# Optimization experiments

Measured on AMD Instinct MI355X. Metric: run time of the kernel, lower is better.

The kernel has to match this reference:

```python
import jax, jax.numpy as jnp
import numpy as np
from jax import lax

B, T, D = 8, 4096, 1024


def setup_inputs() -> dict:
    key = jax.random.key(0)
    ks = jax.random.split(key, 8)
    s = 1.0 / np.sqrt(D)  # keep GEMM outputs O(1)
    return {
        "x": jax.random.normal(ks[0], (B, T, D), dtype=jnp.float32),
        "state_p": jnp.zeros((B, D), dtype=jnp.float32),
        "decay": 0.8 + 0.19 * jax.random.uniform(ks[1], (D,), dtype=jnp.float32),  # ~0.9, stable
        "mass": jnp.ones((D,), dtype=jnp.float32),
        "Wq": s * jax.random.normal(ks[2], (D, D), dtype=jnp.float32),
        "bq": jnp.zeros((D,), dtype=jnp.float32),
        "Wk": s * jax.random.normal(ks[3], (D, D), dtype=jnp.float32),
        "bk": jnp.zeros((D,), dtype=jnp.float32),
        "Wv": s * jax.random.normal(ks[4], (D, D), dtype=jnp.float32),
        "bv": jnp.zeros((D,), dtype=jnp.float32),
    }


def reference(x, state_p, decay, mass, Wq, bq, Wk, bk, Wv, bv):
    # Batch all per-timestep projections into single GEMMs over (B*T) tokens.
    k_logit = jnp.einsum("btd,ed->bte", x, Wk) + bk        # [B,T,D]
    v = jnp.einsum("btd,ed->bte", x, Wv) + bv              # [B,T,D]
    u = jax.nn.sigmoid(k_logit) * v                          # gated input, [B,T,D]

    # Diagonal linear recurrence p_t = decay * p_{t-1} + u_t via scan over time.
    def step(p, u_t):
        p = p * decay + u_t
        return p, p

    final_p, ps = lax.scan(step, state_p, jnp.swapaxes(u, 0, 1))  # ps: [T,B,D]
    p = jnp.swapaxes(ps, 0, 1)                                     # [B,T,D]

    velocities = (jnp.einsum("btd,ed->bte", p, Wq) + bq) / mass    # [B,T,D]
    return velocities, final_p
```

## Files before the change

### kernel.cpp

```cpp
#include <hip/hip_runtime.h>
#include <stdint.h>
#include <stddef.h>

#define D_DIM 1024
#define T_LEN 4096
#define B_SZ 8
#define M_ROWS 32768
#define KTOT 1024
#define CHUNK 64
#define NCHUNK 64

typedef unsigned short u16;
typedef unsigned short u16x8 __attribute__((ext_vector_type(8)));
typedef __bf16 bf16x8 __attribute__((ext_vector_type(8)));
typedef float f32x4 __attribute__((ext_vector_type(4)));

__device__ __forceinline__ u16 f2bf(float f) {
    union { float f; unsigned u; } v; v.f = f;
    unsigned r = v.u + 0x7fffu + ((v.u >> 16) & 1u);
    return (u16)(r >> 16);
}
__device__ __forceinline__ float bf2f(u16 h) {
    union { unsigned u; float f; } v; v.u = ((unsigned)h) << 16;
    return v.f;
}

__global__ void convert_kernel(const float* __restrict__ src, u16* __restrict__ dst, int n4) {
    int i = blockIdx.x * blockDim.x + threadIdx.x;
    int stride = gridDim.x * blockDim.x;
    for (int j = i; j < n4; j += stride) {
        float4 v = ((const float4*)src)[j];
        ushort4 o;
        o.x = f2bf(v.x); o.y = f2bf(v.y); o.z = f2bf(v.z); o.w = f2bf(v.w);
        ((ushort4*)dst)[j] = o;
    }
}

__global__ void convert3_kernel(const float* __restrict__ s0, const float* __restrict__ s1,
                                const float* __restrict__ s2,
                                u16* __restrict__ d0, u16* __restrict__ d1, u16* __restrict__ d2,
                                int n4each) {
    int i = blockIdx.x * blockDim.x + threadIdx.x;
    int total = 3 * n4each;
    int stride = gridDim.x * blockDim.x;
    for (int j = i; j < total; j += stride) {
        int which = j / n4each;
        int off = j - which * n4each;
        const float* s = which == 0 ? s0 : (which == 1 ? s1 : s2);
        u16* d = which == 0 ? d0 : (which == 1 ? d1 : d2);
        float4 v = ((const float4*)s)[off];
        ushort4 o;
        o.x = f2bf(v.x); o.y = f2bf(v.y); o.z = f2bf(v.z); o.w = f2bf(v.w);
        ((ushort4*)d)[off] = o;
    }
}

__device__ __forceinline__ void gload16(const u16* g, u16* l) {
    __builtin_amdgcn_global_load_lds(
        (const __attribute__((address_space(1))) void*)g,
        (__attribute__((address_space(3))) void*)l,
        16, 0, 0);
}

template<bool DUAL>
__global__ __launch_bounds__(512, 2) void gemm3_kernel(
    const u16* __restrict__ A,
    const u16* __restrict__ B0g,
    const u16* __restrict__ B1g,
    const float* __restrict__ bias0,
    const float* __restrict__ bias1,
    u16* __restrict__ Uout,
    float* __restrict__ Fout)
{
    constexpr int BM = 256;
    constexpr int BN = DUAL ? 128 : 256;
    constexpr int MFR = DUAL ? 4 : 8;
    constexpr int BUF = 16384;
    constexpr int NT = KTOT / 32;

    __shared__ u16 smem[4 * BUF];

    const int tid  = threadIdx.x;
    const int w    = tid >> 6;
    const int lane = tid & 63;

    const int cpx = gridDim.x >> 3;
    const int bid = blockIdx.x;
    const int swz = (bid & 7) * cpx + (bid >> 3);

    const int nCol = D_DIM / BN;
    const int M0 = (swz / nCol) * BM;
    const int N0 = (swz % nCol) * BM / (BM / BN);

    const int srow  = lane >> 2;
    const int sslot = lane & 3;
    const int sg    = sslot ^ ((srow >> 1) & 3);

    const u16* pA0 = A + (size_t)(M0 + (w * 2 + 0) * 16 + srow) * KTOT + sg * 8;
    const u16* pA1 = A + (size_t)(M0 + (w * 2 + 1) * 16 + srow) * KTOT + sg * 8;
    const u16* pB0a;
    const u16* pB0b = nullptr;
    const u16* pB1a = nullptr;
    if (DUAL) {
        pB0a = B0g + (size_t)(N0 + w * 16 + srow) * KTOT + sg * 8;
        pB1a = B1g + (size_t)(N0 + w * 16 + srow) * KTOT + sg * 8;
    } else {
        pB0a = B0g + (size_t)(N0 + (w * 2 + 0) * 16 + srow) * KTOT + sg * 8;
        pB0b = B0g + (size_t)(N0 + (w * 2 + 1) * 16 + srow) * KTOT + sg * 8;
    }

    auto stageA = [&](int buf) {
        u16* s = smem + buf * BUF;
        gload16(pA0, s + (w * 2 + 0) * 512); pA0 += 32;
        gload16(pA1, s + (w * 2 + 1) * 512); pA1 += 32;
    };
    auto stageB = [&](int buf) {
        u16* s = smem + buf * BUF;
        if (DUAL) {
            gload16(pB0a, s + 8192 + w * 512);  pB0a += 32;
            gload16(pB1a, s + 12288 + w * 512); pB1a += 32;
        } else {
            gload16(pB0a, s + 8192 + (w * 2 + 0) * 512); pB0a += 32;
            gload16(pB0b, s + 8192 + (w * 2 + 1) * 512); pB0b += 32;
        }
    };

    const int wrow = DUAL ? (w >> 1) * 64 : (w >> 2) * 128;
    const int wcol = DUAL ? (w & 1) * 64 : (w & 3) * 64;
    const int fr = lane & 15;
    const int fq = lane >> 4;

    int offA[MFR], offB[4];
#pragma unroll
    for (int m = 0; m < MFR; ++m) {
        int row = wrow + m * 16 + fr;
        offA[m] = row * 32 + ((fq ^ ((row >> 1) & 3)) << 3);
    }
#pragma unroll
    for (int n = 0; n < 4; ++n) {
        int row = wcol + n * 16 + fr;
        offB[n] = row * 32 + ((fq ^ ((row >> 1) & 3)) << 3);
    }

    f32x4 acc0[MFR][4] = {};
    f32x4 acc1[DUAL ? MFR : 1][4] = {};

    stageA(0); stageB(0); stageA(1); stageB(1); stageA(2); stageB(2);

    for (int kt = 0; kt < NT; ++kt) {
        if (kt < NT - 2)       asm volatile("s_waitcnt vmcnt(8)" ::: "memory");
        else if (kt == NT - 2) asm volatile("s_waitcnt vmcnt(4)" ::: "memory");
        else                   asm volatile("s_waitcnt vmcnt(0)" ::: "memory");
        __builtin_amdgcn_s_barrier();

        const u16* As  = smem + (kt & 3) * BUF;
        const u16* Bs0 = As + 8192;
        const u16* Bs1 = As + 12288;

        bf16x8 af[MFR], b0f[4], b1f[4];

#pragma unroll
        for (int m = 0; m < 4; ++m)
            af[m] = *(const bf16x8*)(As + offA[m]);
#pragma unroll
        for (int n = 0; n < 4; ++n)
            b0f[n] = *(const bf16x8*)(Bs0 + offB[n]);
        if (kt + 3 < NT) stageA((kt + 3) & 3);
        asm volatile("s_waitcnt lgkmcnt(0)" ::: "memory");
        __builtin_amdgcn_sched_barrier(0);
        __builtin_amdgcn_s_setprio(1);
#pragma unroll
        for (int m = 0; m < 4; ++m)
#pragma unroll
            for (int n = 0; n < 4; ++n)
                acc0[m][n] = __builtin_amdgcn_mfma_f32_16x16x32_bf16(af[m], b0f[n], acc0[m][n], 0, 0, 0);
        __builtin_amdgcn_s_setprio(0);
        __builtin_amdgcn_sched_barrier(0);

        __builtin_amdgcn_s_barrier();
        if (DUAL) {
#pragma unroll
            for (int n = 0; n < 4; ++n)
                b1f[n] = *(const bf16x8*)(Bs1 + offB[n]);
        } else {
#pragma unroll
            for (int m = 4; m < MFR; ++m)
                af[m] = *(const bf16x8*)(As + offA[m]);
        }
        if (kt + 3 < NT) stageB((kt + 3) & 3);
        asm volatile("s_waitcnt lgkmcnt(0)" ::: "memory");
        __builtin_amdgcn_sched_barrier(0);
        __builtin_amdgcn_s_setprio(1);
        if (DUAL) {
#pragma unroll
            for (int m = 0; m < 4; ++m)
#pragma unroll
                for (int n = 0; n < 4; ++n)
                    acc1[m][n] = __builtin_amdgcn_mfma_f32_16x16x32_bf16(af[m], b1f[n], acc1[m][n], 0, 0, 0);
        } else {
#pragma unroll
            for (int m = 4; m < MFR; ++m)
#pragma unroll
                for (int n = 0; n < 4; ++n)
                    acc0[m][n] = __builtin_amdgcn_mfma_f32_16x16x32_bf16(af[m], b0f[n], acc0[m][n], 0, 0, 0);
        }
        __builtin_amdgcn_s_setprio(0);
        __builtin_amdgcn_sched_barrier(0);
    }

#pragma unroll
    for (int n = 0; n < 4; ++n) {
        int col = N0 + wcol + n * 16 + fr;
        float b0 = bias0[col];
        float b1 = bias1[col];
#pragma unroll
        for (int m = 0; m < MFR; ++m) {
            int row0 = M0 + wrow + m * 16 + fq * 4;
#pragma unroll
            for (int j = 0; j < 4; ++j) {
                if (DUAL) {
                    float kl = acc0[m][n][j] + b0;
                    float vv = acc1[m][n][j] + b1;
                    float sg2 = 1.0f / (1.0f + __expf(-kl));
                    Uout[(size_t)(row0 + j) * D_DIM + col] = f2bf(sg2 * vv);
                } else {
                    Fout[(size_t)(row0 + j) * D_DIM + col] = (acc0[m][n][j] + b0) / b1;
                }
            }
        }
    }
}

__global__ void chunk_carry_kernel(const u16* __restrict__ u, const float* __restrict__ decay,
                                   float* __restrict__ localc) {
    int id = blockIdx.x * blockDim.x + threadIdx.x;
    int d8 = id & 127;
    int c  = (id >> 7) & (NCHUNK - 1);
    int b  = id >> 13;
    float4 dlo = ((const float4*)decay)[d8 * 2];
    float4 dhi = ((const float4*)decay)[d8 * 2 + 1];
    float dec[8] = {dlo.x, dlo.y, dlo.z, dlo.w, dhi.x, dhi.y, dhi.z, dhi.w};
    float carry[8] = {};
    const u16* up = u + ((size_t)b * T_LEN + (size_t)c * CHUNK) * D_DIM + d8 * 8;
    for (int s = 0; s < CHUNK; ++s) {
        u16x8 v = *(const u16x8*)(up + (size_t)s * D_DIM);
#pragma unroll
        for (int j = 0; j < 8; ++j)
            carry[j] = fmaf(carry[j], dec[j], bf2f(v[j]));
    }
    float* lc = localc + ((size_t)(b * NCHUNK + c)) * D_DIM + d8 * 8;
#pragma unroll
    for (int j = 0; j < 8; ++j) lc[j] = carry[j];
}

__global__ void carry_scan_kernel(const float* __restrict__ localc, const float* __restrict__ state_p,
                                  const float* __restrict__ decay, float* __restrict__ prefix,
                                  float* __restrict__ final_p) {
    int id = blockIdx.x * blockDim.x + threadIdx.x;
    int d = id & (D_DIM - 1);
    int b = id >> 10;
    float dec = decay[d];
    float dl = dec;
#pragma unroll
    for (int i = 0; i < 6; ++i) dl *= dl;
    float P = state_p[id];
    for (int c = 0; c < NCHUNK; ++c) {
        int idx = (b * NCHUNK + c) * D_DIM + d;
        prefix[idx] = P;
        P = fmaf(P, dl, localc[idx]);
    }
    final_p[id] = P;
}

__global__ void reconstruct_kernel(u16* __restrict__ u, const float* __restrict__ decay,
                                   const float* __restrict__ prefix) {
    int id = blockIdx.x * blockDim.x + threadIdx.x;
    int d8 = id & 127;
    int c  = (id >> 7) & (NCHUNK - 1);
    int b  = id >> 13;
    float4 dlo = ((const float4*)decay)[d8 * 2];
    float4 dhi = ((const float4*)decay)[d8 * 2 + 1];
    float dec[8] = {dlo.x, dlo.y, dlo.z, dlo.w, dhi.x, dhi.y, dhi.z, dhi.w};
    const float* pf = prefix + ((size_t)(b * NCHUNK + c)) * D_DIM + d8 * 8;
    float p[8];
#pragma unroll
    for (int j = 0; j < 8; ++j) p[j] = pf[j];
    u16* up = u + ((size_t)b * T_LEN + (size_t)c * CHUNK) * D_DIM + d8 * 8;
    for (int s = 0; s < CHUNK; ++s) {
        u16x8 v = *(const u16x8*)(up + (size_t)s * D_DIM);
        u16x8 o;
#pragma unroll
        for (int j = 0; j < 8; ++j) {
            p[j] = fmaf(p[j], dec[j], bf2f(v[j]));
            o[j] = f2bf(p[j]);
        }
        *(u16x8*)(up + (size_t)s * D_DIM) = o;
    }
}

extern "C" void kernel_launch(void* const* d_in, const int* in_sizes, int n_in,
                              void* d_out, int out_size, void* d_ws, size_t ws_size,
                              hipStream_t stream) {
    const float* x       = (const float*)d_in[0];
    const float* state_p = (const float*)d_in[1];
    const float* decay   = (const float*)d_in[2];
    const float* mass    = (const float*)d_in[3];
    const float* Wq      = (const float*)d_in[4];
    const float* bq      = (const float*)d_in[5];
    const float* Wk      = (const float*)d_in[6];
    const float* bk      = (const float*)d_in[7];
    const float* Wv      = (const float*)d_in[8];
    const float* bv      = (const float*)d_in[9];

    float* out     = (float*)d_out;
    float* final_p = out + (size_t)M_ROWS * D_DIM;

    u16* xb = (u16*)d_out;

    u16* wkb = (u16*)d_ws;
    u16* wvb = wkb + 1048576;
    u16* wqb = wvb + 1048576;
    u16* ub  = wqb + 1048576;
    float* localc = (float*)(ub + (size_t)M_ROWS * D_DIM);
    float* prefix = localc + B_SZ * NCHUNK * D_DIM;

    convert_kernel<<<4096, 256, 0, stream>>>(x, xb, (M_ROWS * D_DIM) / 4);
    convert3_kernel<<<1024, 256, 0, stream>>>(Wk, Wv, Wq, wkb, wvb, wqb, (D_DIM * D_DIM) / 4);

    gemm3_kernel<true><<<dim3(1024), dim3(512), 0, stream>>>(
        xb, wkb, wvb, bk, bv, ub, nullptr);

    chunk_carry_kernel<<<256, 256, 0, stream>>>(ub, decay, localc);
    carry_scan_kernel<<<32, 256, 0, stream>>>(localc, state_p, decay, prefix, final_p);
    reconstruct_kernel<<<256, 256, 0, stream>>>(ub, decay, prefix);

    gemm3_kernel<false><<<dim3(512), dim3(512), 0, stream>>>(
        ub, wqb, nullptr, bq, mass, nullptr, out);
}
```

Measured before the change: 306.4 us.

## Software-pipeline LDS fragment loads across k-steps with ping-pong register buffers

Restructures the GEMM main loop so the A and B0 fragments for the next k-tile are read from LDS during the current tile's second MFMA phase. Two register sets alternate between tiles, and partial lgkmcnt waits replace full drains. The goal is to hide LDS read latency behind MFMA work. In exchange it raises register pressure under launch_bounds(512,2), and the vmcnt and barrier ordering changes could race if miscounted.

```diff
diff --git a/kernel.cpp b/kernel.cpp
--- a/kernel.cpp
+++ b/kernel.cpp
@@ -63,7 +63,7 @@
 }
 
 template<bool DUAL>
-__global__ __launch_bounds__(512, 2) void gemm3_kernel(
+__global__ __launch_bounds__(512, 2) void gemm4_kernel(
     const u16* __restrict__ A,
     const u16* __restrict__ B0g,
     const u16* __restrict__ B1g,
@@ -90,7 +90,7 @@
 
     const int nCol = D_DIM / BN;
     const int M0 = (swz / nCol) * BM;
-    const int N0 = (swz % nCol) * BM / (BM / BN);
+    const int N0 = (swz % nCol) * BN;
 
     const int srow  = lane >> 2;
     const int sslot = lane & 3;
@@ -143,70 +143,75 @@
     }
 
     f32x4 acc0[MFR][4] = {};
-    f32x4 acc1[DUAL ? MFR : 1][4] = {};
+    f32x4 acc1[DUAL ? 4 : 1][4] = {};
+    bf16x8 af0[MFR], af1[MFR], b00[4], b01[4];
+    bf16x8 b1f[DUAL ? 4 : 1];
 
     stageA(0); stageB(0); stageA(1); stageB(1); stageA(2); stageB(2);
-
-    for (int kt = 0; kt < NT; ++kt) {
-        if (kt < NT - 2)       asm volatile("s_waitcnt vmcnt(8)" ::: "memory");
-        else if (kt == NT - 2) asm volatile("s_waitcnt vmcnt(4)" ::: "memory");
-        else                   asm volatile("s_waitcnt vmcnt(0)" ::: "memory");
-        __builtin_amdgcn_s_barrier();
-
-        const u16* As  = smem + (kt & 3) * BUF;
-        const u16* Bs0 = As + 8192;
-        const u16* Bs1 = As + 12288;
-
-        bf16x8 af[MFR], b0f[4], b1f[4];
-
-#pragma unroll
-        for (int m = 0; m < 4; ++m)
-            af[m] = *(const bf16x8*)(As + offA[m]);
-#pragma unroll
-        for (int n = 0; n < 4; ++n)
-            b0f[n] = *(const bf16x8*)(Bs0 + offB[n]);
-        if (kt + 3 < NT) stageA((kt + 3) & 3);
-        asm volatile("s_waitcnt lgkmcnt(0)" ::: "memory");
-        __builtin_amdgcn_sched_barrier(0);
-        __builtin_amdgcn_s_setprio(1);
-#pragma unroll
-        for (int m = 0; m < 4; ++m)
-#pragma unroll
-            for (int n = 0; n < 4; ++n)
-                acc0[m][n] = __builtin_amdgcn_mfma_f32_16x16x32_bf16(af[m], b0f[n], acc0[m][n], 0, 0, 0);
-        __builtin_amdgcn_s_setprio(0);
-        __builtin_amdgcn_sched_barrier(0);
-
-        __builtin_amdgcn_s_barrier();
-        if (DUAL) {
-#pragma unroll
-            for (int n = 0; n < 4; ++n)
-                b1f[n] = *(const bf16x8*)(Bs1 + offB[n]);
-        } else {
-#pragma unroll
-            for (int m = 4; m < MFR; ++m)
-                af[m] = *(const bf16x8*)(As + offA[m]);
-        }
-        if (kt + 3 < NT) stageB((kt + 3) & 3);
-        asm volatile("s_waitcnt lgkmcnt(0)" ::: "memory");
-        __builtin_amdgcn_sched_barrier(0);
-        __builtin_amdgcn_s_setprio(1);
-        if (DUAL) {
-#pragma unroll
-            for (int m = 0; m < 4; ++m)
-#pragma unroll
-                for (int n = 0; n < 4; ++n)
-                    acc1[m][n] = __builtin_amdgcn_mfma_f32_16x16x32_bf16(af[m], b1f[n], acc1[m][n], 0, 0, 0);
-        } else {
-#pragma unroll
-            for (int m = 4; m < MFR; ++m)
-#pragma unroll
-                for (int n = 0; n < 4; ++n)
-                    acc0[m][n] = __builtin_amdgcn_mfma_f32_16x16x32_bf16(af[m], b0f[n], acc0[m][n], 0, 0, 0);
-        }
-        __builtin_amdgcn_s_setprio(0);
-        __builtin_amdgcn_sched_barrier(0);
-    }
+    asm volatile("s_waitcnt vmcnt(8)" ::: "memory");
+    __builtin_amdgcn_s_barrier();
+#pragma unroll
+    for (int m = 0; m < 4; ++m) af0[m] = *(const bf16x8*)(smem + offA[m]);
+#pragma unroll
+    for (int n = 0; n < 4; ++n) b00[n] = *(const bf16x8*)(smem + 8192 + offB[n]);
+
+#define PHASES(KT, AFC, B0C, AFN, B0N)                                               \
+  {                                                                                  \
+    const int kt_ = (KT);                                                            \
+    if (kt_ < NT - 2) { asm volatile("s_waitcnt vmcnt(4)" ::: "memory"); }           \
+    else              { asm volatile("s_waitcnt vmcnt(0)" ::: "memory"); }           \
+    __builtin_amdgcn_sched_barrier(0);                                               \
+    const u16* As_ = smem + (kt_ & 3) * BUF;                                         \
+    if constexpr (DUAL) {                                                            \
+      _Pragma("unroll") for (int n = 0; n < 4; ++n)                                  \
+        b1f[n] = *(const bf16x8*)(As_ + 12288 + offB[n]);                            \
+    } else {                                                                         \
+      _Pragma("unroll") for (int m = 4; m < MFR; ++m)                                \
+        AFC[m] = *(const bf16x8*)(As_ + offA[m]);                                    \
+    }                                                                                \
+    if (kt_ + 3 < NT) stageA((kt_ + 3) & 3);                                         \
+    __builtin_amdgcn_sched_barrier(0);                                               \
+    __builtin_amdgcn_s_barrier();                                                    \
+    asm volatile("s_waitcnt lgkmcnt(4)" ::: "memory");                               \
+    __builtin_amdgcn_sched_barrier(0);                                               \
+    __builtin_amdgcn_s_setprio(1);                                                   \
+    _Pragma("unroll") for (int m = 0; m < 4; ++m)                                    \
+      _Pragma("unroll") for (int n = 0; n < 4; ++n)                                  \
+        acc0[m][n] = __builtin_amdgcn_mfma_f32_16x16x32_bf16(AFC[m], B0C[n], acc0[m][n], 0, 0, 0); \
+    __builtin_amdgcn_s_setprio(0);                                                   \
+    __builtin_amdgcn_sched_barrier(0);                                               \
+    __builtin_amdgcn_s_barrier();                                                    \
+    const u16* Asn_ = smem + ((kt_ + 1) & 3) * BUF;                                  \
+    _Pragma("unroll") for (int m = 0; m < 4; ++m)                                    \
+      AFN[m] = *(const bf16x8*)(Asn_ + offA[m]);                                     \
+    _Pragma("unroll") for (int n = 0; n < 4; ++n)                                    \
+      B0N[n] = *(const bf16x8*)(Asn_ + 8192 + offB[n]);                              \
+    if (kt_ + 3 < NT) stageB((kt_ + 3) & 3);                                         \
+    __builtin_amdgcn_sched_barrier(0);                                               \
+    __builtin_amdgcn_s_barrier();                                                    \
+    asm volatile("s_waitcnt lgkmcnt(8)" ::: "memory");                               \
+    __builtin_amdgcn_sched_barrier(0);                                               \
+    __builtin_amdgcn_s_setprio(1);                                                   \
+    if constexpr (DUAL) {                                                            \
+      _Pragma("unroll") for (int m = 0; m < 4; ++m)                                  \
+        _Pragma("unroll") for (int n = 0; n < 4; ++n)                                \
+          acc1[m][n] = __builtin_amdgcn_mfma_f32_16x16x32_bf16(AFC[m], b1f[n], acc1[m][n], 0, 0, 0); \
+    } else {                                                                         \
+      _Pragma("unroll") for (int m = 4; m < MFR; ++m)                                \
+        _Pragma("unroll") for (int n = 0; n < 4; ++n)                                \
+          acc0[m][n] = __builtin_amdgcn_mfma_f32_16x16x32_bf16(AFC[m], B0C[n], acc0[m][n], 0, 0, 0); \
+    }                                                                                \
+    __builtin_amdgcn_s_setprio(0);                                                   \
+    __builtin_amdgcn_sched_barrier(0);                                               \
+    __builtin_amdgcn_s_barrier();                                                    \
+  }
+
+#pragma unroll 1
+    for (int kt = 0; kt < NT; kt += 2) {
+        PHASES(kt,     af0, b00, af1, b01);
+        PHASES(kt + 1, af1, b01, af0, b00);
+    }
+#undef PHASES
 
 #pragma unroll
     for (int n = 0; n < 4; ++n) {
@@ -327,13 +332,13 @@
     convert_kernel<<<4096, 256, 0, stream>>>(x, xb, (M_ROWS * D_DIM) / 4);
     convert3_kernel<<<1024, 256, 0, stream>>>(Wk, Wv, Wq, wkb, wvb, wqb, (D_DIM * D_DIM) / 4);
 
-    gemm3_kernel<true><<<dim3(1024), dim3(512), 0, stream>>>(
+    gemm4_kernel<true><<<dim3(1024), dim3(512), 0, stream>>>(
         xb, wkb, wvb, bk, bv, ub, nullptr);
 
     chunk_carry_kernel<<<256, 256, 0, stream>>>(ub, decay, localc);
     carry_scan_kernel<<<32, 256, 0, stream>>>(localc, state_p, decay, prefix, final_p);
     reconstruct_kernel<<<256, 256, 0, stream>>>(ub, decay, prefix);
 
-    gemm3_kernel<false><<<dim3(512), dim3(512), 0, stream>>>(
+    gemm4_kernel<false><<<dim3(512), dim3(512), 0, stream>>>(
         ub, wqb, nullptr, bq, mass, nullptr, out);
 }
```

Result: no change. 310.4 us (+1.3%).

## Interleave Wk/Wv into one weight matrix and use a 64-deep double-buffered GEMM

Applied to the files above, without the earlier changes.

Wk and Wv are interleaved in 16-row groups into one concatenated bf16 weight matrix. The first GEMM then runs as a single 256x256 tile GEMM whose epilogue pairs adjacent k/v fragments to apply sigmoid gating, replacing the separate dual-B path. The GEMM pipeline changes from a 4-stage, 32-wide K buffer ring to 2 buffers of 64-wide K, split into four half-steps with more barriers. This is meant to cut barrier/wait overhead per K element and unify tile shapes, but it trades prefetch depth for larger stages, which risks exposing memory latency.

```diff
diff --git a/kernel.cpp b/kernel.cpp
--- a/kernel.cpp
+++ b/kernel.cpp
@@ -36,22 +36,26 @@
     }
 }
 
-__global__ void convert3_kernel(const float* __restrict__ s0, const float* __restrict__ s1,
-                                const float* __restrict__ s2,
-                                u16* __restrict__ d0, u16* __restrict__ d1, u16* __restrict__ d2,
-                                int n4each) {
-    int i = blockIdx.x * blockDim.x + threadIdx.x;
-    int total = 3 * n4each;
+__global__ void convert_w_kernel(const float* __restrict__ Wk, const float* __restrict__ Wv,
+                                 const float* __restrict__ Wq,
+                                 u16* __restrict__ wcat, u16* __restrict__ wqb) {
+    int total = 3072 * 256;
     int stride = gridDim.x * blockDim.x;
-    for (int j = i; j < total; j += stride) {
-        int which = j / n4each;
-        int off = j - which * n4each;
-        const float* s = which == 0 ? s0 : (which == 1 ? s1 : s2);
-        u16* d = which == 0 ? d0 : (which == 1 ? d1 : d2);
-        float4 v = ((const float4*)s)[off];
+    for (int idx = blockIdx.x * blockDim.x + threadIdx.x; idx < total; idx += stride) {
+        int r = idx >> 8, c4 = idx & 255;
+        const float* src; u16* dst;
+        if (r < 2048) {
+            int g = r >> 5, j = r & 31;
+            src = (j < 16 ? Wk : Wv) + (size_t)(g * 16 + (j & 15)) * D_DIM;
+            dst = wcat + (size_t)r * D_DIM;
+        } else {
+            src = Wq + (size_t)(r - 2048) * D_DIM;
+            dst = wqb + (size_t)(r - 2048) * D_DIM;
+        }
+        float4 v = ((const float4*)src)[c4];
         ushort4 o;
         o.x = f2bf(v.x); o.y = f2bf(v.y); o.z = f2bf(v.z); o.w = f2bf(v.w);
-        ((ushort4*)d)[off] = o;
+        ((ushort4*)dst)[c4] = o;
     }
 }
 
@@ -62,110 +66,98 @@
         16, 0, 0);
 }
 
-template<bool DUAL>
-__global__ __launch_bounds__(512, 2) void gemm3_kernel(
+template<bool CAT>
+__global__ __launch_bounds__(512, 2) void gemm5_kernel(
     const u16* __restrict__ A,
-    const u16* __restrict__ B0g,
-    const u16* __restrict__ B1g,
+    const u16* __restrict__ Bg,
     const float* __restrict__ bias0,
     const float* __restrict__ bias1,
     u16* __restrict__ Uout,
     float* __restrict__ Fout)
 {
-    constexpr int BM = 256;
-    constexpr int BN = DUAL ? 128 : 256;
-    constexpr int MFR = DUAL ? 4 : 8;
-    constexpr int BUF = 16384;
-    constexpr int NT = KTOT / 32;
-
-    __shared__ u16 smem[4 * BUF];
+    constexpr int NT = KTOT / 64;
+    __shared__ u16 smem[2 * 32768];
 
     const int tid  = threadIdx.x;
     const int w    = tid >> 6;
     const int lane = tid & 63;
 
     const int cpx = gridDim.x >> 3;
-    const int bid = blockIdx.x;
-    const int swz = (bid & 7) * cpx + (bid >> 3);
-
-    const int nCol = D_DIM / BN;
-    const int M0 = (swz / nCol) * BM;
-    const int N0 = (swz % nCol) * BM / (BM / BN);
-
-    const int srow  = lane >> 2;
-    const int sslot = lane & 3;
-    const int sg    = sslot ^ ((srow >> 1) & 3);
-
-    const u16* pA0 = A + (size_t)(M0 + (w * 2 + 0) * 16 + srow) * KTOT + sg * 8;
-    const u16* pA1 = A + (size_t)(M0 + (w * 2 + 1) * 16 + srow) * KTOT + sg * 8;
-    const u16* pB0a;
-    const u16* pB0b = nullptr;
-    const u16* pB1a = nullptr;
-    if (DUAL) {
-        pB0a = B0g + (size_t)(N0 + w * 16 + srow) * KTOT + sg * 8;
-        pB1a = B1g + (size_t)(N0 + w * 16 + srow) * KTOT + sg * 8;
-    } else {
-        pB0a = B0g + (size_t)(N0 + (w * 2 + 0) * 16 + srow) * KTOT + sg * 8;
-        pB0b = B0g + (size_t)(N0 + (w * 2 + 1) * 16 + srow) * KTOT + sg * 8;
-    }
-
-    auto stageA = [&](int buf) {
-        u16* s = smem + buf * BUF;
-        gload16(pA0, s + (w * 2 + 0) * 512); pA0 += 32;
-        gload16(pA1, s + (w * 2 + 1) * 512); pA1 += 32;
+    const int swz = (blockIdx.x & 7) * cpx + (blockIdx.x >> 3);
+    const int nCol = CAT ? 8 : 4;
+    const int M0 = (swz / nCol) * 256;
+    const int N0 = (swz % nCol) * 256;
+
+    const int srow = lane >> 2;
+    const int sg   = (lane & 3) ^ ((srow >> 1) & 3);
+
+    const u16* pA0 = A  + (size_t)(M0 + w * 32 +      srow) * KTOT + sg * 8;
+    const u16* pA1 = A  + (size_t)(M0 + w * 32 + 16 + srow) * KTOT + sg * 8;
+    const u16* pB0 = Bg + (size_t)(N0 + w * 32 +      srow) * KTOT + sg * 8;
+    const u16* pB1 = Bg + (size_t)(N0 + w * 32 + 16 + srow) * KTOT + sg * 8;
+
+    auto stA = [&](u16* nxt, int h) {
+        gload16(pA0, nxt + h * 8192 + w * 1024);       pA0 += 32;
+        gload16(pA1, nxt + h * 8192 + w * 1024 + 512); pA1 += 32;
     };
-    auto stageB = [&](int buf) {
-        u16* s = smem + buf * BUF;
-        if (DUAL) {
-            gload16(pB0a, s + 8192 + w * 512);  pB0a += 32;
-            gload16(pB1a, s + 12288 + w * 512); pB1a += 32;
-        } else {
-            gload16(pB0a, s + 8192 + (w * 2 + 0) * 512); pB0a += 32;
-            gload16(pB0b, s + 8192 + (w * 2 + 1) * 512); pB0b += 32;
-        }
+    auto stB = [&](u16* nxt, int h) {
+        gload16(pB0, nxt + 16384 + h * 8192 + w * 1024);       pB0 += 32;
+        gload16(pB1, nxt + 16384 + h * 8192 + w * 1024 + 512); pB1 += 32;
     };
 
-    const int wrow = DUAL ? (w >> 1) * 64 : (w >> 2) * 128;
-    const int wcol = DUAL ? (w & 1) * 64 : (w & 3) * 64;
+    const int wrow = (w >> 2) * 128;
+    const int wcol = (w & 3) * 64;
     const int fr = lane & 15;
     const int fq = lane >> 4;
 
-    int offA[MFR], offB[4];
-#pragma unroll
-    for (int m = 0; m < MFR; ++m) {
+    int offA[8], offB[4];
+#pragma unroll
+    for (int m = 0; m < 8; ++m) {
         int row = wrow + m * 16 + fr;
         offA[m] = row * 32 + ((fq ^ ((row >> 1) & 3)) << 3);
     }
 #pragma unroll
     for (int n = 0; n < 4; ++n) {
         int row = wcol + n * 16 + fr;
-        offB[n] = row * 32 + ((fq ^ ((row >> 1) & 3)) << 3);
-    }
-
-    f32x4 acc0[MFR][4] = {};
-    f32x4 acc1[DUAL ? MFR : 1][4] = {};
-
-    stageA(0); stageB(0); stageA(1); stageB(1); stageA(2); stageB(2);
-
-    for (int kt = 0; kt < NT; ++kt) {
-        if (kt < NT - 2)       asm volatile("s_waitcnt vmcnt(8)" ::: "memory");
-        else if (kt == NT - 2) asm volatile("s_waitcnt vmcnt(4)" ::: "memory");
-        else                   asm volatile("s_waitcnt vmcnt(0)" ::: "memory");
-        __builtin_amdgcn_s_barrier();
-
-        const u16* As  = smem + (kt & 3) * BUF;
-        const u16* Bs0 = As + 8192;
-        const u16* Bs1 = As + 12288;
-
-        bf16x8 af[MFR], b0f[4], b1f[4];
-
+        offB[n] = 16384 + row * 32 + ((fq ^ ((row >> 1) & 3)) << 3);
+    }
+
+    f32x4 acc[8][4] = {};
+
+    stA(smem, 0); stB(smem, 0); stA(smem, 1); stB(smem, 1);
+    asm volatile("s_waitcnt vmcnt(4)" ::: "memory");
+    __builtin_amdgcn_s_barrier();
+
+#pragma unroll 1
+    for (int t = 0; t < NT; ++t) {
+        const u16* cur = smem + (t & 1) * 32768;
+        u16* nxt = smem + ((t + 1) & 1) * 32768;
+        const bool pf = (t + 1 < NT);
+
+        bf16x8 aA[4], aB[4], bA[4], aC[4], aD[4], bC[4];
+
+#pragma unroll
+        for (int n = 0; n < 4; ++n) bA[n] = *(const bf16x8*)(cur + offB[n]);
+#pragma unroll
+        for (int m = 0; m < 4; ++m) aA[m] = *(const bf16x8*)(cur + offA[m]);
+        if (pf) stA(nxt, 0);
+        __builtin_amdgcn_s_barrier();
+        asm volatile("s_waitcnt lgkmcnt(0)" ::: "memory");
+        __builtin_amdgcn_sched_barrier(0);
+        __builtin_amdgcn_s_setprio(1);
 #pragma unroll
         for (int m = 0; m < 4; ++m)
-            af[m] = *(const bf16x8*)(As + offA[m]);
-#pragma unroll
-        for (int n = 0; n < 4; ++n)
-            b0f[n] = *(const bf16x8*)(Bs0 + offB[n]);
-        if (kt + 3 < NT) stageA((kt + 3) & 3);
+#pragma unroll
+            for (int n = 0; n < 4; ++n)
+                acc[m][n] = __builtin_amdgcn_mfma_f32_16x16x32_bf16(aA[m], bA[n], acc[m][n], 0, 0, 0);
+        __builtin_amdgcn_s_setprio(0);
+        __builtin_amdgcn_sched_barrier(0);
+        __builtin_amdgcn_s_barrier();
+
+#pragma unroll
+        for (int m = 0; m < 4; ++m) aB[m] = *(const bf16x8*)(cur + offA[4 + m]);
+        if (pf) stB(nxt, 0);
+        __builtin_amdgcn_s_barrier();
         asm volatile("s_waitcnt lgkmcnt(0)" ::: "memory");
         __builtin_amdgcn_sched_barrier(0);
         __builtin_amdgcn_s_setprio(1);
@@ -173,59 +165,80 @@
         for (int m = 0; m < 4; ++m)
 #pragma unroll
             for (int n = 0; n < 4; ++n)
-                acc0[m][n] = __builtin_amdgcn_mfma_f32_16x16x32_bf16(af[m], b0f[n], acc0[m][n], 0, 0, 0);
+                acc[4 + m][n] = __builtin_amdgcn_mfma_f32_16x16x32_bf16(aB[m], bA[n], acc[4 + m][n], 0, 0, 0);
         __builtin_amdgcn_s_setprio(0);
         __builtin_amdgcn_sched_barrier(0);
-
-        __builtin_amdgcn_s_barrier();
-        if (DUAL) {
+        if (pf) { asm volatile("s_waitcnt vmcnt(4)" ::: "memory"); }
+        else    { asm volatile("s_waitcnt vmcnt(0)" ::: "memory"); }
+        __builtin_amdgcn_s_barrier();
+
+#pragma unroll
+        for (int n = 0; n < 4; ++n) bC[n] = *(const bf16x8*)(cur + 8192 + offB[n]);
+#pragma unroll
+        for (int m = 0; m < 4; ++m) aC[m] = *(const bf16x8*)(cur + 8192 + offA[m]);
+        if (pf) stA(nxt, 1);
+        __builtin_amdgcn_s_barrier();
+        asm volatile("s_waitcnt lgkmcnt(0)" ::: "memory");
+        __builtin_amdgcn_sched_barrier(0);
+        __builtin_amdgcn_s_setprio(1);
+#pragma unroll
+        for (int m = 0; m < 4; ++m)
 #pragma unroll
             for (int n = 0; n < 4; ++n)
-                b1f[n] = *(const bf16x8*)(Bs1 + offB[n]);
-        } else {
-#pragma unroll
-            for (int m = 4; m < MFR; ++m)
-                af[m] = *(const bf16x8*)(As + offA[m]);
+                acc[m][n] = __builtin_amdgcn_mfma_f32_16x16x32_bf16(aC[m], bC[n], acc[m][n], 0, 0, 0);
+        __builtin_amdgcn_s_setprio(0);
+        __builtin_amdgcn_sched_barrier(0);
+        __builtin_amdgcn_s_barrier();
+
+#pragma unroll
+        for (int m = 0; m < 4; ++m) aD[m] = *(const bf16x8*)(cur + 8192 + offA[4 + m]);
+        if (pf) stB(nxt, 1);
+        __builtin_amdgcn_s_barrier();
+        asm volatile("s_waitcnt lgkmcnt(0)" ::: "memory");
+        __builtin_amdgcn_sched_barrier(0);
+        __builtin_amdgcn_s_setprio(1);
+#pragma unroll
+        for (int m = 0; m < 4; ++m)
+#pragma unroll
+            for (int n = 0; n < 4; ++n)
+                acc[4 + m][n] = __builtin_amdgcn_mfma_f32_16x16x32_bf16(aD[m], bC[n], acc[4 + m][n], 0, 0, 0);
+        __builtin_amdgcn_s_setprio(0);
+        __builtin_amdgcn_sched_barrier(0);
+        if (pf) { asm volatile("s_waitcnt vmcnt(4)" ::: "memory"); }
+        __builtin_amdgcn_s_barrier();
+    }
+
+    if (CAT) {
+        const int ucol0 = N0 / 2 + (w & 3) * 32;
+#pragma unroll
+        for (int p = 0; p < 2; ++p) {
+            int col = ucol0 + p * 16 + fr;
+            float b0 = bias0[col];
+            float b1 = bias1[col];
+#pragma unroll
+            for (int m = 0; m < 8; ++m) {
+                int row0 = M0 + wrow + m * 16 + fq * 4;
+#pragma unroll
+                for (int j = 0; j < 4; ++j) {
+                    float kl = acc[m][2 * p][j] + b0;
+                    float vv = acc[m][2 * p + 1][j] + b1;
+                    float sig = 1.0f / (1.0f + __expf(-kl));
+                    Uout[(size_t)(row0 + j) * D_DIM + col] = f2bf(sig * vv);
+                }
+            }
         }
-        if (kt + 3 < NT) stageB((kt + 3) & 3);
-        asm volatile("s_waitcnt lgkmcnt(0)" ::: "memory");
-        __builtin_amdgcn_sched_barrier(0);
-        __builtin_amdgcn_s_setprio(1);
-        if (DUAL) {
-#pragma unroll
-            for (int m = 0; m < 4; ++m)
-#pragma unroll
-                for (int n = 0; n < 4; ++n)
-                    acc1[m][n] = __builtin_amdgcn_mfma_f32_16x16x32_bf16(af[m], b1f[n], acc1[m][n], 0, 0, 0);
-        } else {
-#pragma unroll
-            for (int m = 4; m < MFR; ++m)
-#pragma unroll
-                for (int n = 0; n < 4; ++n)
-                    acc0[m][n] = __builtin_amdgcn_mfma_f32_16x16x32_bf16(af[m], b0f[n], acc0[m][n], 0, 0, 0);
-        }
-        __builtin_amdgcn_s_setprio(0);
-        __builtin_amdgcn_sched_barrier(0);
-    }
-
-#pragma unroll
-    for (int n = 0; n < 4; ++n) {
-        int col = N0 + wcol + n * 16 + fr;
-        float b0 = bias0[col];
-        float b1 = bias1[col];
-#pragma unroll
-        for (int m = 0; m < MFR; ++m) {
-            int row0 = M0 + wrow + m * 16 + fq * 4;
-#pragma unroll
-            for (int j = 0; j < 4; ++j) {
-                if (DUAL) {
-                    float kl = acc0[m][n][j] + b0;
-                    float vv = acc1[m][n][j] + b1;
-                    float sg2 = 1.0f / (1.0f + __expf(-kl));
-                    Uout[(size_t)(row0 + j) * D_DIM + col] = f2bf(sg2 * vv);
-                } else {
-                    Fout[(size_t)(row0 + j) * D_DIM + col] = (acc0[m][n][j] + b0) / b1;
-                }
+    } else {
+#pragma unroll
+        for (int n = 0; n < 4; ++n) {
+            int col = N0 + wcol + n * 16 + fr;
+            float b0 = bias0[col];
+            float b1 = bias1[col];
+#pragma unroll
+            for (int m = 0; m < 8; ++m) {
+                int row0 = M0 + wrow + m * 16 + fq * 4;
+#pragma unroll
+                for (int j = 0; j < 4; ++j)
+                    Fout[(size_t)(row0 + j) * D_DIM + col] = (acc[m][n][j] + b0) / b1;
             }
         }
     }
@@ -317,23 +330,22 @@
 
     u16* xb = (u16*)d_out;
 
-    u16* wkb = (u16*)d_ws;
-    u16* wvb = wkb + 1048576;
-    u16* wqb = wvb + 1048576;
-    u16* ub  = wqb + 1048576;
+    u16* wcat = (u16*)d_ws;
+    u16* wqb  = wcat + 2048 * 1024;
+    u16* ub   = wqb + 1024 * 1024;
     float* localc = (float*)(ub + (size_t)M_ROWS * D_DIM);
     float* prefix = localc + B_SZ * NCHUNK * D_DIM;
 
     convert_kernel<<<4096, 256, 0, stream>>>(x, xb, (M_ROWS * D_DIM) / 4);
-    convert3_kernel<<<1024, 256, 0, stream>>>(Wk, Wv, Wq, wkb, wvb, wqb, (D_DIM * D_DIM) / 4);
-
-    gemm3_kernel<true><<<dim3(1024), dim3(512), 0, stream>>>(
-        xb, wkb, wvb, bk, bv, ub, nullptr);
+    convert_w_kernel<<<1536, 256, 0, stream>>>(Wk, Wv, Wq, wcat, wqb);
+
+    gemm5_kernel<true><<<dim3(1024), dim3(512), 0, stream>>>(
+        xb, wcat, bk, bv, ub, nullptr);
 
     chunk_carry_kernel<<<256, 256, 0, stream>>>(ub, decay, localc);
     carry_scan_kernel<<<32, 256, 0, stream>>>(localc, state_p, decay, prefix, final_p);
     reconstruct_kernel<<<256, 256, 0, stream>>>(ub, decay, prefix);
 
-    gemm3_kernel<false><<<dim3(512), dim3(512), 0, stream>>>(
-        ub, wqb, nullptr, bq, mass, nullptr, out);
-}
+    gemm5_kernel<false><<<dim3(512), dim3(512), 0, stream>>>(
+        ub, wqb, bq, mass, nullptr, out);
+}
```

Measured after the change: 309.0 us. No clear change (+0.9%).
